# Performance work log

Measured on AMD Instinct MI355X. Metric: run time of the kernel, lower is better.

Reference implementation:

```python
import jax, jax.numpy as jnp
import numpy as np

B, H, W, C = 8, 128, 128, 192
NH, WS, SHIFT = 6, 8, 4
N = WS * WS          # tokens per window = 64
NWIN = (H // WS) * (W // WS)  # 256 windows per image
SCALE = (C // NH) ** -0.5
EPS = 1e-5

# ---- relative position index (static, numpy) ----
_c = np.stack(np.meshgrid(np.arange(WS), np.arange(WS), indexing='ij')).reshape(2, -1)
_r = (_c[:, :, None] - _c[:, None, :]).transpose(1, 2, 0).astype(np.int64)
_r[..., 0] += WS - 1
_r[..., 1] += WS - 1
_r[..., 0] *= 2 * WS - 1
REL_IDX = jnp.asarray(_r.sum(-1))  # (N, N) in [0, (2*WS-1)**2)

# ---- shifted-window attention mask (static, numpy) ----
_img = np.zeros((H, W))
_cnt = 0
for hs in (slice(0, -WS), slice(-WS, -SHIFT), slice(-SHIFT, None)):
    for ws_ in (slice(0, -WS), slice(-WS, -SHIFT), slice(-SHIFT, None)):
        _img[hs, ws_] = _cnt
        _cnt += 1
_img = _img.reshape(H // WS, WS, W // WS, WS).transpose(0, 2, 1, 3).reshape(-1, N)
_m = _img[:, None, :] - _img[:, :, None]
ATTN_MASK = jnp.asarray(np.where(_m != 0, -100.0, 0.0).astype(np.float32))  # (NWIN, N, N)


def layer_norm(x, w, b):
    mu = x.mean(-1, keepdims=True)
    var = ((x - mu) ** 2).mean(-1, keepdims=True)  # biased variance
    return (x - mu) / jnp.sqrt(var + EPS) * w + b


def window_partition(x):
    # (B, H, W, C) -> (B*NWIN, N, C)
    x = x.reshape(B, H // WS, WS, W // WS, WS, C)
    return x.transpose(0, 1, 3, 2, 4, 5).reshape(B * NWIN, N, C)


def window_reverse(w_):
    # (B*NWIN, N, C) -> (B, H, W, C)
    x = w_.reshape(B, H // WS, W // WS, WS, WS, C)
    return x.transpose(0, 1, 3, 2, 4, 5).reshape(B, H, W, C)


def setup_inputs() -> dict:
    key = jax.random.key(0)
    ks = jax.random.split(key, 6)
    return {
        'x': jax.random.normal(ks[0], (B, H * W, C), jnp.float32),
        'ln1_w': jnp.ones((C,), jnp.float32),
        'ln1_b': jnp.zeros((C,), jnp.float32),
        'qkv_w': jax.random.normal(ks[1], (C, 3 * C), jnp.float32) * 0.02,
        'qkv_b': jnp.zeros((3 * C,), jnp.float32),
        'rpb_table': jax.random.normal(ks[2], ((2 * WS - 1) ** 2, NH), jnp.float32) * 0.02,
        'proj_w': jax.random.normal(ks[3], (C, C), jnp.float32) * 0.02,
        'proj_b': jnp.zeros((C,), jnp.float32),
        'ln2_w': jnp.ones((C,), jnp.float32),
        'ln2_b': jnp.zeros((C,), jnp.float32),
        'fc1_w': jax.random.normal(ks[4], (C, 4 * C), jnp.float32) * 0.02,
        'fc1_b': jnp.zeros((4 * C,), jnp.float32),
        'fc2_w': jax.random.normal(ks[5], (4 * C, C), jnp.float32) * 0.02,
        'fc2_b': jnp.zeros((C,), jnp.float32),
    }


def reference(x, ln1_w, ln1_b, qkv_w, qkv_b, rpb_table, proj_w, proj_b,
              ln2_w, ln2_b, fc1_w, fc1_b, fc2_w, fc2_b):
    shortcut = x
    h = layer_norm(x, ln1_w, ln1_b).reshape(B, H, W, C)
    # cyclic shift
    h = jnp.roll(h, shift=(-SHIFT, -SHIFT), axis=(1, 2))
    xw = window_partition(h)  # (B*NWIN, N, C)

    qkv = (xw @ qkv_w + qkv_b).reshape(B * NWIN, N, 3, NH, C // NH)
    q, k, v = [qkv[:, :, i].transpose(0, 2, 1, 3) for i in range(3)]  # (Bn, NH, N, hd)
    attn = jnp.einsum('bhqd,bhkd->bhqk', q * SCALE, k)  # (Bn, NH, N, N)

    rel_bias = rpb_table[REL_IDX].transpose(2, 0, 1)  # (NH, N, N)
    attn = attn + rel_bias[None]
    # shift mask: broadcast per window
    attn = attn.reshape(B, NWIN, NH, N, N) + ATTN_MASK[None, :, None]
    attn = jax.nn.softmax(attn.reshape(B * NWIN, NH, N, N), axis=-1)

    out = jnp.einsum('bhqk,bhkd->bhqd', attn, v)
    out = out.transpose(0, 2, 1, 3).reshape(B * NWIN, N, C)
    out = out @ proj_w + proj_b

    h = window_reverse(out)
    h = jnp.roll(h, shift=(SHIFT, SHIFT), axis=(1, 2)).reshape(B, H * W, C)
    x = shortcut + h

    # MLP
    m = layer_norm(x, ln2_w, ln2_b)
    m = jax.nn.gelu(m @ fc1_w + fc1_b, approximate=False) @ fc2_w + fc2_b
    return x + m
```

## Files before the change

kernel.cpp:

```cpp
#include <hip/hip_runtime.h>
#include <math.h>

typedef _Float16 f16;
typedef _Float16 f16x8 __attribute__((ext_vector_type(8)));
typedef float f32x4 __attribute__((ext_vector_type(4)));

namespace {
constexpr int Hh = 128, Ww = 128, Cc = 192;
constexpr int NHh = 6;
constexpr int Nn = 64, HDd = 32;
constexpr int SH = 4;
constexpr int Mrows = 131072;
constexpr int NWINtot = 2048;
constexpr float LNEPS = 1e-5f;
constexpr float QSCALE = 0.17677669529663687f;
}

__device__ __forceinline__ void ldsload16(const void* g, void* l) {
  __builtin_amdgcn_global_load_lds(
      (const __attribute__((address_space(1))) void*)g,
      (__attribute__((address_space(3))) void*)l, 16, 0, 0);
}

__device__ __forceinline__ int win_row_to_src(int m) {
  int tok = m & 63;
  int wi  = m >> 6;
  int ww = wi & 15, wh = (wi >> 4) & 15, b = wi >> 8;
  int r = (wh << 3) + (tok >> 3);
  int c = (ww << 3) + (tok & 7);
  int ro = (r + SH) & (Hh - 1);
  int co = (c + SH) & (Ww - 1);
  return (b << 14) + (ro << 7) + co;
}

template <int GATHER>
__global__ __launch_bounds__(256) void ln_prep_kernel(
    const float* __restrict__ X, const float* __restrict__ lnw,
    const float* __restrict__ lnb, f16* __restrict__ outh, int m0) {
  __shared__ float xr[16][192];
  __shared__ float smu[16], srs[16];
  __shared__ int src[16];
  const int t = threadIdx.x;
  const int r0 = blockIdx.x * 16;
  if (t < 16) {
    int m = m0 + r0 + t;
    src[t] = GATHER ? win_row_to_src(m) : m;
  }
  __syncthreads();
#pragma unroll
  for (int it = 0; it < 3; ++it) {
    int f = t + it * 256;
    int row = f / 48, c4 = f - row * 48;
    float4 v = *(const float4*)&X[(size_t)src[row] * 192 + c4 * 4];
    *(float4*)&xr[row][c4 * 4] = v;
  }
  __syncthreads();
  {
    const int lane = t & 63, w = t >> 6;
    const int g = lane >> 4, li = lane & 15;
    const int row = w * 4 + g;
    float s = 0.f, s2 = 0.f;
#pragma unroll
    for (int j = 0; j < 12; ++j) {
      float v = xr[row][li + j * 16];
      s += v; s2 += v * v;
    }
#pragma unroll
    for (int off = 1; off < 16; off <<= 1) {
      s += __shfl_xor(s, off);
      s2 += __shfl_xor(s2, off);
    }
    if (li == 0) {
      float m = s * (1.f / 192.f);
      smu[row] = m;
      srs[row] = rsqrtf(s2 * (1.f / 192.f) - m * m + LNEPS);
    }
  }
  __syncthreads();
#pragma unroll
  for (int it = 0; it < 2; ++it) {
    int c = t + it * 256;
    if (c < 384) {
      int e0 = c * 8;
      int row = e0 / 192, col = e0 - row * 192;
      float mu_ = smu[row], rs_ = srs[row];
      f16x8 o;
#pragma unroll
      for (int j = 0; j < 8; ++j) {
        float v = (xr[row][col + j] - mu_) * rs_ * lnw[col + j] + lnb[col + j];
        o[j] = (f16)v;
      }
      *(f16x8*)&outh[(size_t)(m0 + r0) * 192 + e0] = o;
    }
  }
}

__global__ __launch_bounds__(256) void rpb_expand_kernel(
    const float* __restrict__ rpb, float* __restrict__ biasF2) {
  int t = blockIdx.x * 256 + threadIdx.x;
  if (t >= NHh * 4 * 4 * 64 * 4) return;
  int r = t & 3, lane = (t >> 2) & 63, jt = (t >> 8) & 3, it = (t >> 10) & 3, h = t >> 12;
  int row = it * 16 + (lane >> 4) * 4 + r;
  int col = jt * 16 + (lane & 15);
  int dh = (row >> 3) - (col >> 3) + 7;
  int dw = (row & 7) - (col & 7) + 7;
  biasF2[t] = rpb[(dh * 15 + dw) * NHh + h];
}

__global__ __launch_bounds__(256) void wconv_frag(
    const float* __restrict__ W, f16* __restrict__ Wf, int K, int N) {
  int tid = blockIdx.x * 256 + threadIdx.x;
  if (tid >= K * N) return;
  int e = tid & 7, lane = (tid >> 3) & 63, f = tid >> 9;
  int NKT = K >> 5;
  int kt = f % NKT, nt = f / NKT;
  int k = kt * 32 + ((lane >> 4) << 3) + e;
  int n = nt * 16 + (lane & 15);
  Wf[tid] = (f16)W[(size_t)k * N + n];
}

template <int KDIM, int NDIM, int EMODE>
__global__ __launch_bounds__(512, 2) void gemm_mfma16(
    const f16* __restrict__ Abase, const f16* __restrict__ Bf,
    const float* __restrict__ bias, const float* __restrict__ resid,
    void* __restrict__ outp, int m0a, int m0e, int nbx) {
  constexpr int NCH = KDIM / 192;
  constexpr int NKT = KDIM / 32;
  __shared__ __align__(16) char lds[48 * 1024];

  const int tid = threadIdx.x;
  const int lane = tid & 63;
  const int wid = tid >> 6;
  const int wr = wid & 1, wc = wid >> 1;
  const int l15 = lane & 15, g2 = lane >> 4;

  int b = blockIdx.x;
  const int nb = gridDim.x;
  if ((nb & 7) == 0) b = (b & 7) * (nb >> 3) + (b >> 3);
  const int bx = b % nbx;
  const int by = b / nbx;
  const int bn = bx * 192;
  const int bm = by * 128;
  const int nt0 = bx * 12 + wc * 3;

  const int srow = tid >> 2;
  const int kq = tid & 3;
  const int sg = srow >> 4;
  const int slot = srow & 15;
  const f16* arow = Abase + (size_t)(m0a + bm + srow) * KDIM;

  f32x4 acc[4][3];
#pragma unroll
  for (int i = 0; i < 4; ++i)
#pragma unroll
    for (int j = 0; j < 3; ++j) acc[i][j] = (f32x4){0.f, 0.f, 0.f, 0.f};

  for (int c = 0; c < NCH; ++c) {
    if (c) __syncthreads();
#pragma unroll
    for (int u = 0; u < 6; ++u) {
      int ch = kq + u * 4;
      f16x8 v = *(const f16x8*)&arow[c * 192 + ch * 8];
      int ks = ch >> 2, h = ch & 3;
      *(f16x8*)(lds + (ks * 8 + sg) * 1024 + (slot + h * 16) * 16) = v;
    }
    __syncthreads();

#pragma unroll
    for (int ks = 0; ks < 6; ++ks) {
      f16x8 bf[3];
#pragma unroll
      for (int ni = 0; ni < 3; ++ni)
        bf[ni] = *(const f16x8*)&Bf[
            (((size_t)(nt0 + ni) * NKT + (c * 6 + ks)) << 9) + (lane << 3)];
#pragma unroll
      for (int mi = 0; mi < 4; ++mi) {
        f16x8 ah = *(const f16x8*)(lds + (ks * 8 + wr * 4 + mi) * 1024 + lane * 16);
#pragma unroll
        for (int ni = 0; ni < 3; ++ni)
          acc[mi][ni] = __builtin_amdgcn_mfma_f32_16x16x32_f16(ah, bf[ni], acc[mi][ni], 0, 0, 0);
      }
    }
  }

#pragma unroll
  for (int mi = 0; mi < 4; ++mi) {
#pragma unroll
    for (int ni = 0; ni < 3; ++ni) {
      int col = bn + wc * 48 + ni * 16 + l15;
      float bcol = bias[col];
#pragma unroll
      for (int r = 0; r < 4; ++r) {
        int ml = bm + wr * 64 + mi * 16 + g2 * 4 + r;
        ((f16*)outp)[(size_t)ml * NDIM + col] = (f16)(acc[mi][ni][r] + bcol);
      }
    }
  }
}

__global__ __launch_bounds__(256, 2) void mlp_fused(
    const f16* __restrict__ W1f, const f16* __restrict__ W2f,
    const float* __restrict__ b1, const float* __restrict__ b2,
    const float* __restrict__ lnw, const float* __restrict__ lnb,
    float* __restrict__ out) {
  __shared__ __align__(16) char ldsA[24 * 1024];
  __shared__ __align__(16) char ldsH[24 * 1024];

  const int tid = threadIdx.x;
  const int lane = tid & 63;
  const int wc = tid >> 6;
  const int l15 = lane & 15, g2 = lane >> 4;
  const int bm = blockIdx.x * 64;

  {
    const float* rowp = out + (size_t)(bm + wc * 16 + l15) * 192 + g2 * 8;
    float vals[48];
    float s = 0.f, s2 = 0.f;
#pragma unroll
    for (int ks = 0; ks < 6; ++ks) {
      float4 a = *(const float4*)&rowp[ks * 32];
      float4 b = *(const float4*)&rowp[ks * 32 + 4];
      float* vp = &vals[ks * 8];
      vp[0] = a.x; vp[1] = a.y; vp[2] = a.z; vp[3] = a.w;
      vp[4] = b.x; vp[5] = b.y; vp[6] = b.z; vp[7] = b.w;
#pragma unroll
      for (int e = 0; e < 8; ++e) { s += vp[e]; s2 += vp[e] * vp[e]; }
    }
    s += __shfl_xor(s, 16);  s2 += __shfl_xor(s2, 16);
    s += __shfl_xor(s, 32);  s2 += __shfl_xor(s2, 32);
    float mu = s * (1.f / 192.f);
    float rs = rsqrtf(s2 * (1.f / 192.f) - mu * mu + LNEPS);
#pragma unroll
    for (int ks = 0; ks < 6; ++ks) {
      f16x8 o;
#pragma unroll
      for (int e = 0; e < 8; ++e) {
        int k = ks * 32 + g2 * 8 + e;
        o[e] = (f16)((vals[ks * 8 + e] - mu) * rs * lnw[k] + lnb[k]);
      }
      *(f16x8*)(ldsA + (ks * 4 + wc) * 1024 + lane * 16) = o;
    }
  }

  f32x4 acc2[4][3];
#pragma unroll
  for (int i = 0; i < 4; ++i)
#pragma unroll
    for (int j = 0; j < 3; ++j) acc2[i][j] = (f32x4){0.f, 0.f, 0.f, 0.f};

  __syncthreads();

  for (int hc = 0; hc < 4; ++hc) {
    f16x8 w1[6][3];
#pragma unroll
    for (int ks = 0; ks < 6; ++ks)
#pragma unroll
      for (int ni = 0; ni < 3; ++ni)
        w1[ks][ni] = *(const f16x8*)&W1f[
            (((size_t)(hc * 12 + wc * 3 + ni) * 6 + ks) << 9) + (lane << 3)];
    f32x4 acc1[4][3];
#pragma unroll
    for (int i = 0; i < 4; ++i)
#pragma unroll
      for (int j = 0; j < 3; ++j) acc1[i][j] = (f32x4){0.f, 0.f, 0.f, 0.f};
#pragma unroll
    for (int ks = 0; ks < 6; ++ks) {
#pragma unroll
      for (int mi = 0; mi < 4; ++mi) {
        f16x8 ah = *(const f16x8*)(ldsA + (ks * 4 + mi) * 1024 + lane * 16);
#pragma unroll
        for (int ni = 0; ni < 3; ++ni)
          acc1[mi][ni] = __builtin_amdgcn_mfma_f32_16x16x32_f16(ah, w1[ks][ni], acc1[mi][ni], 0, 0, 0);
      }
    }
#pragma unroll
    for (int mi = 0; mi < 4; ++mi)
#pragma unroll
      for (int ni = 0; ni < 3; ++ni) {
        float bcol = b1[hc * 192 + wc * 48 + ni * 16 + l15];
#pragma unroll
        for (int r = 0; r < 4; ++r) {
          float v = acc1[mi][ni][r] + bcol;
          float u = v * (1.f + 0.044715f * v * v);
          float ex = __expf(-1.5957691216f * u);
          v = v * __builtin_amdgcn_rcpf(1.f + ex);
          int row = mi * 16 + g2 * 4 + r;
          int col = wc * 48 + ni * 16 + l15;
          *(f16*)(ldsH + ((col >> 5) * 4 + mi) * 1024 +
                  ((row & 15) + ((col >> 3) & 3) * 16) * 16 + (col & 7) * 2) = (f16)v;
        }
      }
    __syncthreads();

    f16x8 w2[6][3];
#pragma unroll
    for (int ks = 0; ks < 6; ++ks)
#pragma unroll
      for (int ni = 0; ni < 3; ++ni)
        w2[ks][ni] = *(const f16x8*)&W2f[
            (((size_t)(wc * 3 + ni) * 24 + hc * 6 + ks) << 9) + (lane << 3)];
#pragma unroll
    for (int ks = 0; ks < 6; ++ks) {
#pragma unroll
      for (int mi = 0; mi < 4; ++mi) {
        f16x8 ah = *(const f16x8*)(ldsH + (ks * 4 + mi) * 1024 + lane * 16);
#pragma unroll
        for (int ni = 0; ni < 3; ++ni)
          acc2[mi][ni] = __builtin_amdgcn_mfma_f32_16x16x32_f16(ah, w2[ks][ni], acc2[mi][ni], 0, 0, 0);
      }
    }
    __syncthreads();
  }

#pragma unroll
  for (int mi = 0; mi < 4; ++mi)
#pragma unroll
    for (int ni = 0; ni < 3; ++ni) {
      int col = wc * 48 + ni * 16 + l15;
      float bcol = b2[col];
#pragma unroll
      for (int r = 0; r < 4; ++r) {
        int ml = bm + mi * 16 + g2 * 4 + r;
        out[(size_t)ml * 192 + col] = acc2[mi][ni][r] + bcol + out[(size_t)ml * 192 + col];
      }
    }
}

__global__ __launch_bounds__(384) void attn_mfma(
    const f16* __restrict__ qkv, const float* __restrict__ biasF2,
    const f16* __restrict__ Wpf, const float* __restrict__ pb_,
    const float* __restrict__ resid, float* __restrict__ out, int w0) {
  __shared__ f16 Vt[192 * 64];
  __shared__ f16 Pb[NHh][32 * 64];
  const int t = threadIdx.x;
  const int h = t >> 6;
  const int lane = t & 63;
  const int g = lane >> 4, l15 = lane & 15;
  int b = blockIdx.x;
  const int nb = gridDim.x;
  if ((nb & 7) == 0) b = (b & 7) * (nb >> 3) + (b >> 3);
  const int wl = b >> 1;
  const int qh = b & 1;
  const f16* base = qkv + (size_t)wl * 64 * 576;

  {
    const f16* vr = base + (size_t)lane * 576 + 384 + h * 32;
    f16x8 vv[4];
#pragma unroll
    for (int u = 0; u < 4; ++u) vv[u] = *(const f16x8*)&vr[u * 8];
    const int c = lane >> 3, e7 = lane & 7;
#pragma unroll
    for (int u = 0; u < 4; ++u)
#pragma unroll
      for (int e = 0; e < 8; ++e) {
        int d = h * 32 + u * 8 + e;
        Vt[d * 64 + ((c ^ e) << 3) + e7] = vv[u][e];
      }
  }

  f16x8 qf[2], kf[4];
#pragma unroll
  for (int it = 0; it < 2; ++it)
    qf[it] = *(const f16x8*)&base[(size_t)(qh * 32 + it * 16 + l15) * 576 + h * 32 + g * 8];
#pragma unroll
  for (int jt = 0; jt < 4; ++jt)
    kf[jt] = *(const f16x8*)&base[(size_t)(jt * 16 + l15) * 576 + 192 + h * 32 + g * 8];

  f32x4 S[2][4];
#pragma unroll
  for (int it = 0; it < 2; ++it)
#pragma unroll
    for (int jt = 0; jt < 4; ++jt) S[it][jt] = (f32x4){0.f, 0.f, 0.f, 0.f};
#pragma unroll
  for (int it = 0; it < 2; ++it)
#pragma unroll
    for (int jt = 0; jt < 4; ++jt)
      S[it][jt] = __builtin_amdgcn_mfma_f32_16x16x32_f16(qf[it], kf[jt], S[it][jt], 0, 0, 0);

  const int wi = (w0 + wl) & 255;
  const int wh = wi >> 4, wwc = wi & 15;
  int regj[4];
#pragma unroll
  for (int jt = 0; jt < 4; ++jt) {
    int col = jt * 16 + l15;
    int rj = wh * 8 + (col >> 3), cj = wwc * 8 + (col & 7);
    regj[jt] = (rj < 120 ? 0 : rj < 124 ? 1 : 2) * 3 + (cj < 120 ? 0 : cj < 124 ? 1 : 2);
  }
#pragma unroll
  for (int it = 0; it < 2; ++it) {
    const int itg = qh * 2 + it;
    int regi[4];
#pragma unroll
    for (int r = 0; r < 4; ++r) {
      int row = itg * 16 + g * 4 + r;
      int ri = wh * 8 + (row >> 3), ci = wwc * 8 + (row & 7);
      regi[r] = (ri < 120 ? 0 : ri < 124 ? 1 : 2) * 3 + (ci < 120 ? 0 : ci < 124 ? 1 : 2);
    }
#pragma unroll
    for (int jt = 0; jt < 4; ++jt) {
      f32x4 bb = *(const f32x4*)&biasF2[(((h * 4 + itg) * 4 + jt) * 64 + lane) * 4];
#pragma unroll
      for (int r = 0; r < 4; ++r) {
        float v = S[it][jt][r] * QSCALE + bb[r];
        if (regi[r] != regj[jt]) v -= 100.f;
        S[it][jt][r] = v;
      }
    }
  }

#pragma unroll
  for (int it = 0; it < 2; ++it) {
#pragma unroll
    for (int r = 0; r < 4; ++r) {
      float m = fmaxf(fmaxf(S[it][0][r], S[it][1][r]), fmaxf(S[it][2][r], S[it][3][r]));
#pragma unroll
      for (int off = 1; off < 16; off <<= 1) m = fmaxf(m, __shfl_xor(m, off));
#pragma unroll
      for (int jt = 0; jt < 4; ++jt) S[it][jt][r] = __expf(S[it][jt][r] - m);
    }
  }

  f16* pb = &Pb[h][0];
#pragma unroll
  for (int it = 0; it < 2; ++it)
#pragma unroll
    for (int jt = 0; jt < 4; ++jt)
#pragma unroll
      for (int r = 0; r < 4; ++r) {
        int row = it * 16 + g * 4 + r;
        int cs = (jt * 2 + (l15 >> 3)) ^ (row & 7);
        pb[row * 64 + cs * 8 + (l15 & 7)] = (f16)S[it][jt][r];
      }

  f32x4 O[2][2], Ssum[2];
#pragma unroll
  for (int it = 0; it < 2; ++it) {
    O[it][0] = (f32x4){0.f, 0.f, 0.f, 0.f};
    O[it][1] = (f32x4){0.f, 0.f, 0.f, 0.f};
    Ssum[it] = (f32x4){0.f, 0.f, 0.f, 0.f};
  }
  f16x8 ones;
#pragma unroll
  for (int e = 0; e < 8; ++e) ones[e] = (f16)1.f;
#pragma unroll
  for (int jh = 0; jh < 2; ++jh) {
    const int csw = ((jh * 4 + g) ^ (l15 & 7)) << 3;
    f16x8 pf[2], vf[2];
#pragma unroll
    for (int it = 0; it < 2; ++it) pf[it] = *(const f16x8*)&pb[(it * 16 + l15) * 64 + csw];
#pragma unroll
    for (int dt = 0; dt < 2; ++dt) vf[dt] = *(const f16x8*)&Vt[(h * 32 + dt * 16 + l15) * 64 + csw];
#pragma unroll
    for (int it = 0; it < 2; ++it) {
      O[it][0] = __builtin_amdgcn_mfma_f32_16x16x32_f16(pf[it], vf[0], O[it][0], 0, 0, 0);
      O[it][1] = __builtin_amdgcn_mfma_f32_16x16x32_f16(pf[it], vf[1], O[it][1], 0, 0, 0);
      Ssum[it] = __builtin_amdgcn_mfma_f32_16x16x32_f16(pf[it], ones, Ssum[it], 0, 0, 0);
    }
  }

  __syncthreads();

  {
    char* Ao = (char*)&Pb[0][0];
#pragma unroll
    for (int it = 0; it < 2; ++it) {
      f32x4 rin;
#pragma unroll
      for (int r = 0; r < 4; ++r) rin[r] = 1.f / Ssum[it][r];
#pragma unroll
      for (int dt = 0; dt < 2; ++dt) {
        int hh = dt * 2 + (l15 >> 3);
        int e = l15 & 7;
#pragma unroll
        for (int r = 0; r < 4; ++r) {
          *(f16*)(Ao + (h * 2 + it) * 1024 + ((g * 4 + r) + hh * 16) * 16 + e * 2) =
              (f16)(O[it][dt][r] * rin[r]);
        }
      }
    }
  }
  __syncthreads();

  {
    const char* Ao = (const char*)&Pb[0][0];
    f32x4 acc[2][2];
#pragma unroll
    for (int i = 0; i < 2; ++i) {
      acc[i][0] = (f32x4){0.f, 0.f, 0.f, 0.f};
      acc[i][1] = (f32x4){0.f, 0.f, 0.f, 0.f};
    }
#pragma unroll
    for (int ks = 0; ks < 6; ++ks) {
      f16x8 bf[2];
#pragma unroll
      for (int ni = 0; ni < 2; ++ni)
        bf[ni] = *(const f16x8*)&Wpf[(((size_t)(h * 2 + ni) * 6 + ks) << 9) + (lane << 3)];
#pragma unroll
      for (int it = 0; it < 2; ++it) {
        f16x8 ah = *(const f16x8*)(Ao + (ks * 2 + it) * 1024 + lane * 16);
#pragma unroll
        for (int ni = 0; ni < 2; ++ni)
          acc[it][ni] = __builtin_amdgcn_mfma_f32_16x16x32_f16(ah, bf[ni], acc[it][ni], 0, 0, 0);
      }
    }
#pragma unroll
    for (int it = 0; it < 2; ++it)
#pragma unroll
      for (int ni = 0; ni < 2; ++ni) {
        int col = h * 32 + ni * 16 + l15;
        float bcol = pb_[col];
#pragma unroll
        for (int r = 0; r < 4; ++r) {
          int ml = qh * 32 + it * 16 + g * 4 + r;
          int dst = win_row_to_src((w0 + wl) * 64 + ml);
          out[(size_t)dst * 192 + col] = acc[it][ni][r] + bcol + resid[(size_t)dst * 192 + col];
        }
      }
  }
}

extern "C" void kernel_launch(void* const* d_in, const int* in_sizes, int n_in,
                              void* d_out, int out_size, void* d_ws, size_t ws_size,
                              hipStream_t stream) {
  const float* x     = (const float*)d_in[0];
  const float* ln1w  = (const float*)d_in[1];
  const float* ln1b  = (const float*)d_in[2];
  const float* qkvw  = (const float*)d_in[3];
  const float* qkvb  = (const float*)d_in[4];
  const float* rpb   = (const float*)d_in[5];
  const float* projw = (const float*)d_in[6];
  const float* projb = (const float*)d_in[7];
  const float* ln2w  = (const float*)d_in[8];
  const float* ln2b  = (const float*)d_in[9];
  const float* fc1w  = (const float*)d_in[10];
  const float* fc1b  = (const float*)d_in[11];
  const float* fc2w  = (const float*)d_in[12];
  const float* fc2b  = (const float*)d_in[13];
  float* out = (float*)d_out;

  char* ws = (char*)d_ws;
  float* biasF2 = (float*)ws;
  f16* qkvwF = (f16*)(ws + 98304);
  f16* projwF = (f16*)(ws + 319488);
  f16* fc1wF = (f16*)(ws + 393216);
  f16* fc2wF = (f16*)(ws + 688128);
  f16* xh    = (f16*)(ws + 983040);
  char* big  = ws + 983040 + 50331648;
  size_t R = ws_size > (size_t)(983040 + 50331648)
                 ? ws_size - (983040 + 50331648) : 0;

  long long wch = (long long)(R / 73728);
  if (wch > NWINtot) wch = NWINtot;
  wch &= ~1LL;
  if (wch < 2) wch = 2;

  wconv_frag<<<432, 256, 0, stream>>>(qkvw, qkvwF, 192, 576);
  wconv_frag<<<144, 256, 0, stream>>>(projw, projwF, 192, 192);
  wconv_frag<<<576, 256, 0, stream>>>(fc1w, fc1wF, 192, 768);
  wconv_frag<<<576, 256, 0, stream>>>(fc2w, fc2wF, 768, 192);
  rpb_expand_kernel<<<96, 256, 0, stream>>>(rpb, biasF2);

  ln_prep_kernel<1><<<Mrows / 16, 256, 0, stream>>>(x, ln1w, ln1b, xh, 0);

  f16* qkvc = (f16*)big;
  for (int w = 0; w < NWINtot; w += (int)wch) {
    int cur = (NWINtot - w < (int)wch) ? (NWINtot - w) : (int)wch;
    int ny = cur * 64 / 128;
    gemm_mfma16<192, 576, 0><<<3 * ny, 512, 0, stream>>>(
        xh, qkvwF, qkvb, nullptr, qkvc, w * 64, 0, 3);
    attn_mfma<<<cur * 2, 384, 0, stream>>>(qkvc, biasF2, projwF, projb, x, out, w);
  }

  mlp_fused<<<Mrows / 64, 256, 0, stream>>>(
      fc1wF, fc2wF, fc1b, fc2b, ln2w, ln2b, out);
}
```

Measured before the change: 352.3 us.

## Software-pipeline MLP hidden chunks with double-buffered LDS hidden tile

The fused MLP kernel now computes the first fc1 chunk up front, then in each iteration interleaves the fc2 MFMAs for the current hidden chunk with the fc1 MFMAs for the next chunk, writing GELU output into a second LDS buffer. This removes one barrier per chunk and gives the scheduler independent MFMA chains to overlap with weight loads. Weights are now loaded per k-step instead of all at once. The cost is 24 KB more LDS per block, which may reduce occupancy below the declared 2 blocks per CU, plus more live accumulators (acc1 and acc2 together), raising register pressure.

```diff
diff --git a/kernel.cpp b/kernel.cpp
--- a/kernel.cpp
+++ b/kernel.cpp
@@ -204,7 +204,7 @@
     const float* __restrict__ lnw, const float* __restrict__ lnb,
     float* __restrict__ out) {
   __shared__ __align__(16) char ldsA[24 * 1024];
-  __shared__ __align__(16) char ldsH[24 * 1024];
+  __shared__ __align__(16) char ldsH[2][24 * 1024];
 
   const int tid = threadIdx.x;
   const int lane = tid & 63;
@@ -250,34 +250,32 @@
 
   __syncthreads();
 
-  for (int hc = 0; hc < 4; ++hc) {
-    f16x8 w1[6][3];
-#pragma unroll
-    for (int ks = 0; ks < 6; ++ks)
+  {
+    f32x4 acc1[4][3];
+#pragma unroll
+    for (int i = 0; i < 4; ++i)
+#pragma unroll
+      for (int j = 0; j < 3; ++j) acc1[i][j] = (f32x4){0.f, 0.f, 0.f, 0.f};
+#pragma unroll
+    for (int ks = 0; ks < 6; ++ks) {
+      f16x8 w1[3];
 #pragma unroll
       for (int ni = 0; ni < 3; ++ni)
-        w1[ks][ni] = *(const f16x8*)&W1f[
-            (((size_t)(hc * 12 + wc * 3 + ni) * 6 + ks) << 9) + (lane << 3)];
-    f32x4 acc1[4][3];
-#pragma unroll
-    for (int i = 0; i < 4; ++i)
-#pragma unroll
-      for (int j = 0; j < 3; ++j) acc1[i][j] = (f32x4){0.f, 0.f, 0.f, 0.f};
-#pragma unroll
-    for (int ks = 0; ks < 6; ++ks) {
+        w1[ni] = *(const f16x8*)&W1f[
+            (((size_t)(0 * 12 + wc * 3 + ni) * 6 + ks) << 9) + (lane << 3)];
 #pragma unroll
       for (int mi = 0; mi < 4; ++mi) {
         f16x8 ah = *(const f16x8*)(ldsA + (ks * 4 + mi) * 1024 + lane * 16);
 #pragma unroll
         for (int ni = 0; ni < 3; ++ni)
-          acc1[mi][ni] = __builtin_amdgcn_mfma_f32_16x16x32_f16(ah, w1[ks][ni], acc1[mi][ni], 0, 0, 0);
+          acc1[mi][ni] = __builtin_amdgcn_mfma_f32_16x16x32_f16(ah, w1[ni], acc1[mi][ni], 0, 0, 0);
       }
     }
 #pragma unroll
     for (int mi = 0; mi < 4; ++mi)
 #pragma unroll
       for (int ni = 0; ni < 3; ++ni) {
-        float bcol = b1[hc * 192 + wc * 48 + ni * 16 + l15];
+        float bcol = b1[0 * 192 + wc * 48 + ni * 16 + l15];
 #pragma unroll
         for (int r = 0; r < 4; ++r) {
           float v = acc1[mi][ni][r] + bcol;
@@ -286,30 +284,79 @@
           v = v * __builtin_amdgcn_rcpf(1.f + ex);
           int row = mi * 16 + g2 * 4 + r;
           int col = wc * 48 + ni * 16 + l15;
-          *(f16*)(ldsH + ((col >> 5) * 4 + mi) * 1024 +
+          *(f16*)(ldsH[0] + ((col >> 5) * 4 + mi) * 1024 +
                   ((row & 15) + ((col >> 3) & 3) * 16) * 16 + (col & 7) * 2) = (f16)v;
         }
       }
-    __syncthreads();
-
-    f16x8 w2[6][3];
-#pragma unroll
-    for (int ks = 0; ks < 6; ++ks)
-#pragma unroll
-      for (int ni = 0; ni < 3; ++ni)
-        w2[ks][ni] = *(const f16x8*)&W2f[
-            (((size_t)(wc * 3 + ni) * 24 + hc * 6 + ks) << 9) + (lane << 3)];
-#pragma unroll
-    for (int ks = 0; ks < 6; ++ks) {
-#pragma unroll
-      for (int mi = 0; mi < 4; ++mi) {
-        f16x8 ah = *(const f16x8*)(ldsH + (ks * 4 + mi) * 1024 + lane * 16);
+  }
+  __syncthreads();
+
+  for (int hc = 0; hc < 4; ++hc) {
+    const char* cur = ldsH[hc & 1];
+    if (hc < 3) {
+      f32x4 acc1[4][3];
+#pragma unroll
+      for (int i = 0; i < 4; ++i)
+#pragma unroll
+        for (int j = 0; j < 3; ++j) acc1[i][j] = (f32x4){0.f, 0.f, 0.f, 0.f};
+#pragma unroll
+      for (int ks = 0; ks < 6; ++ks) {
+        f16x8 w2[3], w1[3];
+#pragma unroll
+        for (int ni = 0; ni < 3; ++ni) {
+          w2[ni] = *(const f16x8*)&W2f[
+              (((size_t)(wc * 3 + ni) * 24 + hc * 6 + ks) << 9) + (lane << 3)];
+          w1[ni] = *(const f16x8*)&W1f[
+              (((size_t)((hc + 1) * 12 + wc * 3 + ni) * 6 + ks) << 9) + (lane << 3)];
+        }
+#pragma unroll
+        for (int mi = 0; mi < 4; ++mi) {
+          f16x8 ah2 = *(const f16x8*)(cur + (ks * 4 + mi) * 1024 + lane * 16);
+#pragma unroll
+          for (int ni = 0; ni < 3; ++ni)
+            acc2[mi][ni] = __builtin_amdgcn_mfma_f32_16x16x32_f16(ah2, w2[ni], acc2[mi][ni], 0, 0, 0);
+          f16x8 ah1 = *(const f16x8*)(ldsA + (ks * 4 + mi) * 1024 + lane * 16);
+#pragma unroll
+          for (int ni = 0; ni < 3; ++ni)
+            acc1[mi][ni] = __builtin_amdgcn_mfma_f32_16x16x32_f16(ah1, w1[ni], acc1[mi][ni], 0, 0, 0);
+        }
+      }
+      char* nb_ = ldsH[(hc + 1) & 1];
+#pragma unroll
+      for (int mi = 0; mi < 4; ++mi)
+#pragma unroll
+        for (int ni = 0; ni < 3; ++ni) {
+          float bcol = b1[(hc + 1) * 192 + wc * 48 + ni * 16 + l15];
+#pragma unroll
+          for (int r = 0; r < 4; ++r) {
+            float v = acc1[mi][ni][r] + bcol;
+            float u = v * (1.f + 0.044715f * v * v);
+            float ex = __expf(-1.5957691216f * u);
+            v = v * __builtin_amdgcn_rcpf(1.f + ex);
+            int row = mi * 16 + g2 * 4 + r;
+            int col = wc * 48 + ni * 16 + l15;
+            *(f16*)(nb_ + ((col >> 5) * 4 + mi) * 1024 +
+                    ((row & 15) + ((col >> 3) & 3) * 16) * 16 + (col & 7) * 2) = (f16)v;
+          }
+        }
+      __syncthreads();
+    } else {
+#pragma unroll
+      for (int ks = 0; ks < 6; ++ks) {
+        f16x8 w2[3];
 #pragma unroll
         for (int ni = 0; ni < 3; ++ni)
-          acc2[mi][ni] = __builtin_amdgcn_mfma_f32_16x16x32_f16(ah, w2[ks][ni], acc2[mi][ni], 0, 0, 0);
-      }
-    }
-    __syncthreads();
+          w2[ni] = *(const f16x8*)&W2f[
+              (((size_t)(wc * 3 + ni) * 24 + hc * 6 + ks) << 9) + (lane << 3)];
+#pragma unroll
+        for (int mi = 0; mi < 4; ++mi) {
+          f16x8 ah2 = *(const f16x8*)(cur + (ks * 4 + mi) * 1024 + lane * 16);
+#pragma unroll
+          for (int ni = 0; ni < 3; ++ni)
+            acc2[mi][ni] = __builtin_amdgcn_mfma_f32_16x16x32_f16(ah2, w2[ni], acc2[mi][ni], 0, 0, 0);
+        }
+      }
+    }
   }
 
 #pragma unroll
```

Result: slower. 404.6 us (+14.9%).
